# Kernel optimization log

Measured on AMD Instinct MI355X. Metric: run time of the kernel, lower is better.

## Reference

```python
import jax, jax.numpy as jnp
import numpy as np

N, E, H, L, IN_DIM, OUT_DIM = 50000, 500000, 128, 6, 3, 9


def _lin_init(k, fi, fo):
    W = jax.random.normal(k, (fi, fo), jnp.float32) / np.sqrt(fi)
    return W, jnp.zeros((fo,), jnp.float32)


def setup_inputs() -> dict:
    key = jax.random.key(0)
    ks = jax.random.split(key, 40)
    inp = {}
    inp['x'] = jax.random.normal(ks[0], (N, IN_DIM), jnp.float32)
    inp['coords'] = jax.random.uniform(ks[1], (N, 3), jnp.float32)
    inp['edge_index'] = jax.random.randint(ks[2], (2, E), 0, N, jnp.int64)
    # encoders
    inp['W_ne1'], inp['b_ne1'] = _lin_init(ks[3], IN_DIM, H)
    inp['W_ne2'], inp['b_ne2'] = _lin_init(ks[4], H, H)
    inp['W_ee1'], inp['b_ee1'] = _lin_init(ks[5], 4, H)
    inp['W_ee2'], inp['b_ee2'] = _lin_init(ks[6], H, H)
    # per-layer params, stacked over L
    def stack(fn):
        Ws, bs = zip(*[fn(l) for l in range(L)])
        return jnp.stack(Ws), jnp.stack(bs)
    inp['We1'], inp['be1'] = stack(lambda l: _lin_init(ks[7 + l], 3 * H, H))
    inp['We2'], inp['be2'] = stack(lambda l: _lin_init(ks[13 + l], H, H))
    inp['Wn1'], inp['bn1'] = stack(lambda l: _lin_init(ks[19 + l], 2 * H, H))
    inp['Wn2'], inp['bn2'] = stack(lambda l: _lin_init(ks[25 + l], H, H))
    inp['ln_g'] = jnp.ones((L, H), jnp.float32)
    inp['ln_b'] = jnp.zeros((L, H), jnp.float32)
    # decoder
    inp['Wd1'], inp['bd1'] = _lin_init(ks[31], H, H)
    inp['Wd2'], inp['bd2'] = _lin_init(ks[32], H, OUT_DIM)
    return inp


def _mlp2(x, W1, b1, W2, b2):
    return jax.nn.silu(x @ W1 + b1) @ W2 + b2


def _layernorm(x, g, b, eps=1e-5):
    m = jnp.mean(x, -1, keepdims=True)
    v = jnp.mean(jnp.square(x - m), -1, keepdims=True)
    return (x - m) / jnp.sqrt(v + eps) * g + b


def reference(x, coords, edge_index,
              W_ne1, b_ne1, W_ne2, b_ne2, W_ee1, b_ee1, W_ee2, b_ee2,
              We1, be1, We2, be2, Wn1, bn1, Wn2, bn2, ln_g, ln_b,
              Wd1, bd1, Wd2, bd2):
    src, dst = edge_index[0], edge_index[1]
    # edge features: relative displacement + distance -> (E,4)
    rel = coords[dst] - coords[src]
    ef = jnp.concatenate([rel, jnp.linalg.norm(rel, axis=-1, keepdims=True)], -1)
    edge_attr = _mlp2(ef, W_ee1, b_ee1, W_ee2, b_ee2)  # (E,H)
    h = _mlp2(x, W_ne1, b_ne1, W_ne2, b_ne2)           # (N,H)
    # in-degree for mean aggregation (PyG mean -> 0 for isolated nodes)
    deg = jax.ops.segment_sum(jnp.ones((E,), h.dtype), dst, num_segments=N)
    denom = jnp.maximum(deg, 1.0)[:, None]
    for l in range(L):
        # message: phi_e(x_i=h[dst], x_j=h[src], e_ij)
        m_in = jnp.concatenate([h[dst], h[src], edge_attr], -1)  # (E,3H)
        msg = _mlp2(m_in, We1[l], be1[l], We2[l], be2[l])        # (E,H)
        agg = jax.ops.segment_sum(msg, dst, num_segments=N) / denom
        upd = _mlp2(jnp.concatenate([h, agg], -1), Wn1[l], bn1[l], Wn2[l], bn2[l])
        h = _layernorm(upd + h, ln_g[l], ln_b[l])
    return _mlp2(h, Wd1, bd1, Wd2, bd2)  # (N,out_dim)
```

## Files before the change

kernel.cpp:

```cpp
#include <hip/hip_runtime.h>

#define NN 50000
#define NE 500000
#define HD 128

typedef _Float16 f16;
typedef _Float16 f16x8 __attribute__((ext_vector_type(8)));
typedef _Float16 f16x4 __attribute__((ext_vector_type(4)));
typedef float f32x4 __attribute__((ext_vector_type(4)));


__device__ __forceinline__ int swz(int r, int c) {
  return r * HD + ((((c >> 3) ^ r) & 15) << 3) + (c & 7);
}

__device__ __forceinline__ float fast_silu(float x) {
  return x * __builtin_amdgcn_rcpf(1.0f + __expf(-x));
}

__device__ __forceinline__ void gemm_wave_g(const f16* A, const f16* __restrict__ Wg,
                                            int wstride, int rowBase, int colBase,
                                            f32x4 acc[2][4]) {
  const int lane = (int)threadIdx.x & 63;
  const int m = lane & 15;
  const int q = lane >> 4;
#pragma unroll
  for (int kc = 0; kc < 4; ++kc) {
    const int pc = (((kc * 4 + q) ^ m) & 15) << 3;
    const int gk = (kc * 4 + q) << 3;
    f16x8 a0 = *(const f16x8*)(A + (rowBase + m) * HD + pc);
    f16x8 a1 = *(const f16x8*)(A + (rowBase + 16 + m) * HD + pc);
#pragma unroll
    for (int ct = 0; ct < 4; ++ct) {
      f16x8 b = *(const f16x8*)(Wg + (colBase + ct * 16 + m) * wstride + gk);
      acc[0][ct] = __builtin_amdgcn_mfma_f32_16x16x32_f16(a0, b, acc[0][ct], 0, 0, 0);
      acc[1][ct] = __builtin_amdgcn_mfma_f32_16x16x32_f16(a1, b, acc[1][ct], 0, 0, 0);
    }
  }
}

__device__ __forceinline__ void gemm_wave_g2(const f16* A, const f16* __restrict__ Wg,
                                             int wstride, int rowBase, int colBase,
                                             f32x4 acc[2][2]) {
  const int lane = (int)threadIdx.x & 63;
  const int m = lane & 15;
  const int q = lane >> 4;
#pragma unroll
  for (int kc = 0; kc < 4; ++kc) {
    const int pc = (((kc * 4 + q) ^ m) & 15) << 3;
    const int gk = (kc * 4 + q) << 3;
    f16x8 a0 = *(const f16x8*)(A + (rowBase + m) * HD + pc);
    f16x8 a1 = *(const f16x8*)(A + (rowBase + 16 + m) * HD + pc);
#pragma unroll
    for (int ct = 0; ct < 2; ++ct) {
      f16x8 b = *(const f16x8*)(Wg + (colBase + ct * 16 + m) * wstride + gk);
      acc[0][ct] = __builtin_amdgcn_mfma_f32_16x16x32_f16(a0, b, acc[0][ct], 0, 0, 0);
      acc[1][ct] = __builtin_amdgcn_mfma_f32_16x16x32_f16(a1, b, acc[1][ct], 0, 0, 0);
    }
  }
}

#define ZACC(acc)                                        \
  {                                                      \
    _Pragma("unroll") for (int zi = 0; zi < 2; ++zi)     \
        _Pragma("unroll") for (int zj = 0; zj < 4; ++zj) \
            acc[zi][zj] = (f32x4){0.f, 0.f, 0.f, 0.f};   \
  }

#define ZACC2(acc)                                       \
  {                                                      \
    _Pragma("unroll") for (int zi = 0; zi < 2; ++zi)     \
        _Pragma("unroll") for (int zj = 0; zj < 2; ++zj) \
            acc[zi][zj] = (f32x4){0.f, 0.f, 0.f, 0.f};   \
  }

template <int TPB>
__device__ __forceinline__ void stage_rows64(const f16* __restrict__ g, long r0,
                                             long lim, f16* lds) {
#pragma unroll
  for (int it = 0; it < 1024 / TPB; ++it) {
    int idx = it * TPB + (int)threadIdx.x;
    int r = idx >> 4, ck = idx & 15;
    f16x8 v = {};
    if (r0 + r < lim) v = *(const f16x8*)(g + (r0 + r) * HD + ck * 8);
    *(f16x8*)(lds + r * HD + (((ck ^ r) & 15) << 3)) = v;
  }
}
template <int TPB>
__device__ __forceinline__ void store_rows64(const f16* lds, f16* __restrict__ g,
                                             long r0, long lim) {
#pragma unroll
  for (int it = 0; it < 1024 / TPB; ++it) {
    int idx = it * TPB + (int)threadIdx.x;
    int r = idx >> 4, ck = idx & 15;
    if (r0 + r < lim)
      *(f16x8*)(g + (r0 + r) * HD + ck * 8) =
          *(const f16x8*)(lds + r * HD + (((ck ^ r) & 15) << 3));
  }
}

struct TJob {
  const float* src;
  f16* dst;
  int idim;
  int odim;
};
struct TJobs {
  TJob j[27];
};

__global__ __launch_bounds__(256) void k_prep(TJobs jobs) {
  int job = blockIdx.x >> 2;
  int part = blockIdx.x & 3;
  TJob J = jobs.j[job];
  int total = J.idim * J.odim;
  for (int idx = part * 256 + (int)threadIdx.x; idx < total; idx += 1024) {
    int o = idx / J.idim;
    int i = idx - o * J.idim;
    J.dst[idx] = (f16)J.src[(long)i * J.odim + o];
  }
}

__global__ __launch_bounds__(128) void k_prep_E(const float* __restrict__ W,
                                                f16* __restrict__ W8) {
  int t = threadIdx.x;
#pragma unroll
  for (int i = 0; i < 8; ++i) W8[t * 8 + i] = (i < 4) ? (f16)W[i * 128 + t] : (f16)0.f;
}

__global__ __launch_bounds__(128) void k_prep_M(const float* __restrict__ Wee2,
                                                const float* __restrict__ b2,
                                                const float* __restrict__ We1,
                                                f16* __restrict__ Mt,
                                                float* __restrict__ cv) {
  __shared__ float col[128];
  int l = blockIdx.x >> 7, o = blockIdx.x & 127;
  int t = threadIdx.x;
  col[t] = We1[((size_t)l * 384 + 256 + t) * 128 + o];
  __syncthreads();
  float s = 0.f;
#pragma unroll 8
  for (int e = 0; e < 128; ++e) s += Wee2[t * 128 + e] * col[e];
  Mt[((size_t)l * 128 + o) * 128 + t] = (f16)s;
  if (t == 0) {
    float c = 0.f;
    for (int e = 0; e < 128; ++e) c += b2[e] * col[e];
    cv[l * 128 + o] = c;
  }
}

__global__ __launch_bounds__(128) void k_prep_Z(const float* __restrict__ We2,
                                                const float* __restrict__ be2,
                                                const float* __restrict__ Wn1,
                                                f16* __restrict__ WZt,
                                                float* __restrict__ bve) {
  __shared__ float col[128];
  int l = blockIdx.x >> 7, o = blockIdx.x & 127;
  int t = threadIdx.x;
  col[t] = Wn1[((size_t)l * 256 + 128 + t) * 128 + o];
  __syncthreads();
  float s = 0.f;
#pragma unroll 8
  for (int j = 0; j < 128; ++j) s += We2[(size_t)l * 128 * 128 + t * 128 + j] * col[j];
  WZt[((size_t)l * 128 + o) * 128 + t] = (f16)s;
  if (t == 0) {
    float c = 0.f;
    for (int j = 0; j < 128; ++j) c += be2[l * 128 + j] * col[j];
    bve[l * 128 + o] = c;
  }
}

__global__ __launch_bounds__(256) void k_hist(const int* __restrict__ dst,
                                              int* __restrict__ count) {
  int e = blockIdx.x * 256 + threadIdx.x;
  if (e < NE) atomicAdd(&count[dst[e]], 1);
}

__global__ __launch_bounds__(1024) void k_scan(const int* __restrict__ count,
                                               int* __restrict__ startA) {
  __shared__ int lds[1024];
  const int CH = 49;
  int t = threadIdx.x;
  int b = t * CH;
  int e = b + CH < NN ? b + CH : NN;
  int s = 0;
  for (int i = b; i < e; ++i) s += count[i];
  lds[t] = s;
  __syncthreads();
  for (int off = 1; off < 1024; off <<= 1) {
    int v = (t >= off) ? lds[t - off] : 0;
    __syncthreads();
    lds[t] += v;
    __syncthreads();
  }
  int run = lds[t] - s;
  for (int i = b; i < e; ++i) {
    startA[i] = run;
    run += count[i];
  }
  if (t == 0) startA[NN] = NE;
}

__global__ __launch_bounds__(256) void k_scatter(const int* __restrict__ src,
                                                 const int* __restrict__ dst,
                                                 const float* __restrict__ coords,
                                                 const int* __restrict__ startA,
                                                 int* __restrict__ cursor,
                                                 int* __restrict__ srcS,
                                                 int* __restrict__ dstS,
                                                 f16* __restrict__ efS) {
  int e = blockIdx.x * 256 + threadIdx.x;
  if (e >= NE) return;
  int s = src[e];
  int n = dst[e];
  int pos = startA[n] + atomicAdd(&cursor[n], 1);
  srcS[pos] = s;
  dstS[pos] = n;
  float rx = coords[n * 3] - coords[s * 3];
  float ry = coords[n * 3 + 1] - coords[s * 3 + 1];
  float rz = coords[n * 3 + 2] - coords[s * 3 + 2];
  float nr = sqrtf(rx * rx + ry * ry + rz * rz);
  f16x8 v = {};
  v[0] = (f16)rx;
  v[1] = (f16)ry;
  v[2] = (f16)rz;
  v[3] = (f16)nr;
  *(f16x8*)(efS + (long)pos * 8) = v;
}

__global__ __launch_bounds__(256, 4) void k_enc_node(
    const float* __restrict__ x, const float* __restrict__ W1,
    const float* __restrict__ b1, const f16* __restrict__ W2t,
    const float* __restrict__ b2, float* __restrict__ h32, f16* __restrict__ h16) {
  __shared__ __align__(16) f16 lds_A[64 * HD];
  __shared__ __align__(16) f16 lds_O[64 * HD];
  float* lds_x = (float*)lds_O;
  long r0 = (long)blockIdx.x * 64;
  int t = threadIdx.x;
  int wv = t >> 6, lane = t & 63, nn = lane & 15, q = lane >> 4;
  int rowBase = (wv >> 1) * 32, colBase = (wv & 1) * 64;

  if (t < 192) {
    long i = r0 * 3 + t;
    lds_x[t] = (i < (long)NN * 3) ? x[i] : 0.f;
  }
  __syncthreads();

  for (int it = 0; it < 32; ++it) {
    int idx = it * 256 + t;
    int r = idx >> 7, c = idx & 127;
    float a = b1[c];
    a += lds_x[r * 3 + 0] * W1[0 * HD + c];
    a += lds_x[r * 3 + 1] * W1[1 * HD + c];
    a += lds_x[r * 3 + 2] * W1[2 * HD + c];
    lds_A[swz(r, c)] = (f16)fast_silu(a);
  }
  __syncthreads();

  f32x4 acc[2][4];
  ZACC(acc);
  gemm_wave_g(lds_A, W2t, HD, rowBase, colBase, acc);
#pragma unroll
  for (int rt = 0; rt < 2; ++rt)
#pragma unroll
    for (int ct = 0; ct < 4; ++ct)
#pragma unroll
      for (int rg = 0; rg < 4; ++rg) {
        int row = rowBase + rt * 16 + q * 4 + rg;
        int col = colBase + ct * 16 + nn;
        float v = acc[rt][ct][rg] + b2[col];
        long nr = r0 + row;
        if (nr < NN) h32[nr * HD + col] = v;
        lds_O[swz(row, col)] = (f16)v;
      }
  __syncthreads();
  store_rows64<256>(lds_O, h16, r0, NN);
}

__global__ __launch_bounds__(512, 8) void k_pp(const f16* __restrict__ h16,
                                               const f16* __restrict__ We1t,
                                               const float* __restrict__ be1,
                                               const float* __restrict__ cvec,
                                               f16* __restrict__ Pd,
                                               f16* __restrict__ Ps) {
  __shared__ __align__(16) f16 lds_A[64 * HD];
  __shared__ __align__(16) f16 lds_O[64 * HD];
  long r0 = (long)blockIdx.x * 64;
  int t = threadIdx.x;
  int wv = t >> 6, lane = t & 63, nn = lane & 15, q = lane >> 4;
  int rowBase = (wv >> 2) * 32, colBase = (wv & 3) * 32;

  stage_rows64<512>(h16, r0, NN, lds_A);
  __syncthreads();

  f32x4 acc[2][2];
  ZACC2(acc);
  gemm_wave_g2(lds_A, We1t, 384, rowBase, colBase, acc);
#pragma unroll
  for (int rt = 0; rt < 2; ++rt)
#pragma unroll
    for (int ct = 0; ct < 2; ++ct)
#pragma unroll
      for (int rg = 0; rg < 4; ++rg) {
        int row = rowBase + rt * 16 + q * 4 + rg;
        int col = colBase + ct * 16 + nn;
        lds_O[swz(row, col)] = (f16)(acc[rt][ct][rg] + be1[col] + cvec[col]);
      }
  __syncthreads();
  store_rows64<512>(lds_O, Pd, r0, NN);

  ZACC2(acc);
  gemm_wave_g2(lds_A, We1t + 128, 384, rowBase, colBase, acc);
  __syncthreads();
#pragma unroll
  for (int rt = 0; rt < 2; ++rt)
#pragma unroll
    for (int ct = 0; ct < 2; ++ct)
#pragma unroll
      for (int rg = 0; rg < 4; ++rg) {
        int row = rowBase + rt * 16 + q * 4 + rg;
        int col = colBase + ct * 16 + nn;
        lds_O[swz(row, col)] = (f16)acc[rt][ct][rg];
      }
  __syncthreads();
  store_rows64<512>(lds_O, Ps, r0, NN);
}

__global__ __launch_bounds__(512, 8) void k_edge(
    const f16* __restrict__ efS, const int* __restrict__ srcS,
    const int* __restrict__ dstS, const f16* __restrict__ Pd,
    const f16* __restrict__ Ps, const f16* __restrict__ W1e8,
    const float* __restrict__ b1, const f16* __restrict__ Mt,
    float* __restrict__ zs, int nwg) {
  __shared__ __align__(16) f16 lds_A[64 * HD];
  __shared__ __align__(16) f16 lds_P[64 * HD];
  __shared__ int dstL[64];
  int orig = blockIdx.x;
  int xcd = orig & 7, loc = orig >> 3;
  int qq = nwg >> 3, rr = nwg & 7;
  int wg = (xcd < rr ? xcd * (qq + 1) : rr * (qq + 1) + (xcd - rr) * qq) + loc;
  long e0 = (long)wg * 64;
  int t = threadIdx.x;
  int lane = t & 63, nn = lane & 15, q = lane >> 4;
  int wv = t >> 6;
  int rowBase = (wv >> 2) * 32, colBase = (wv & 3) * 32;

  if (t < 64) {
    long e = e0 + t;
    dstL[t] = (e < NE) ? dstS[e] : -1;
  }

  f16x8 ea0 = {}, ea1 = {}, eb0 = {}, eb1 = {};
  if (q == 0) {
    long er0 = e0 + rowBase + nn;
    long er1 = er0 + 16;
    if (er0 < NE) ea0 = *(const f16x8*)(efS + er0 * 8);
    if (er1 < NE) ea1 = *(const f16x8*)(efS + er1 * 8);
    eb0 = *(const f16x8*)(W1e8 + (colBase + nn) * 8);
    eb1 = *(const f16x8*)(W1e8 + (colBase + 16 + nn) * 8);
  }
  f32x4 sacc[2][2];
  ZACC2(sacc);
  sacc[0][0] = __builtin_amdgcn_mfma_f32_16x16x32_f16(ea0, eb0, sacc[0][0], 0, 0, 0);
  sacc[1][0] = __builtin_amdgcn_mfma_f32_16x16x32_f16(ea1, eb0, sacc[1][0], 0, 0, 0);
  sacc[0][1] = __builtin_amdgcn_mfma_f32_16x16x32_f16(ea0, eb1, sacc[0][1], 0, 0, 0);
  sacc[1][1] = __builtin_amdgcn_mfma_f32_16x16x32_f16(ea1, eb1, sacc[1][1], 0, 0, 0);

  int rr0 = t >> 4, rr1 = 32 + (t >> 4);
  int ck = t & 15;
  f16x8 pa0 = {}, pb0 = {}, pa1 = {}, pb1 = {};
  {
    long e = e0 + rr0;
    if (e < NE) {
      int d = dstS[e], s = srcS[e];
      pa0 = *(const f16x8*)(Pd + (long)d * HD + ck * 8);
      pb0 = *(const f16x8*)(Ps + (long)s * HD + ck * 8);
    }
  }
  {
    long e = e0 + rr1;
    if (e < NE) {
      int d = dstS[e], s = srcS[e];
      pa1 = *(const f16x8*)(Pd + (long)d * HD + ck * 8);
      pb1 = *(const f16x8*)(Ps + (long)s * HD + ck * 8);
    }
  }

  {
    float b1v0 = b1[colBase + nn], b1v1 = b1[colBase + 16 + nn];
#pragma unroll
    for (int rt = 0; rt < 2; ++rt)
#pragma unroll
      for (int ct = 0; ct < 2; ++ct) {
        float bb = ct ? b1v1 : b1v0;
        int col = colBase + ct * 16 + nn;
#pragma unroll
        for (int rg = 0; rg < 4; ++rg) {
          int row = rowBase + rt * 16 + q * 4 + rg;
          lds_A[swz(row, col)] = (f16)fast_silu(sacc[rt][ct][rg] + bb);
        }
      }
  }
  {
    f16x8 v = pa0 + pb0;
    *(f16x8*)(lds_P + rr0 * HD + (((ck ^ rr0) & 15) << 3)) = v;
  }
  {
    f16x8 v = pa1 + pb1;
    *(f16x8*)(lds_P + rr1 * HD + (((ck ^ rr1) & 15) << 3)) = v;
  }
  __syncthreads();

  f32x4 acc[2][2];
  ZACC2(acc);
  gemm_wave_g2(lds_A, Mt, HD, rowBase, colBase, acc);

#pragma unroll
  for (int rt = 0; rt < 2; ++rt)
#pragma unroll
    for (int ct = 0; ct < 2; ++ct)
#pragma unroll
      for (int rg = 0; rg < 4; ++rg) {
        int row = rowBase + rt * 16 + q * 4 + rg;
        int col = colBase + ct * 16 + nn;
        float v = acc[rt][ct][rg] + (float)lds_P[swz(row, col)];
        lds_P[swz(row, col)] = (f16)fast_silu(v);
      }
  __syncthreads();

  {
    int c = t & 127, qt = t >> 7;
    int rb = qt * 16;
    int dfirst = dstL[rb], dlast = dstL[rb + 15];
    int prev = dfirst;
    float sum = 0.f;
    for (int r = rb; r < rb + 16; ++r) {
      int d = dstL[r];
      if (d != prev) {
        if (prev >= 0) {
          if (prev == dfirst || prev == dlast)
            atomicAdd(&zs[(long)prev * HD + c], sum);
          else
            zs[(long)prev * HD + c] = sum;
        }
        sum = 0.f;
        prev = d;
      }
      sum += (float)lds_P[swz(r, c)];
    }
    if (prev >= 0) atomicAdd(&zs[(long)prev * HD + c], sum);
  }
}

__global__ __launch_bounds__(256, 4) void k_node(
    const f16* __restrict__ h16in, float* __restrict__ zsum,
    const int* __restrict__ startA, const f16* __restrict__ Wn1t,
    const float* __restrict__ bn1, const f16* __restrict__ WZt,
    const float* __restrict__ bve, const f16* __restrict__ Wn2t,
    const float* __restrict__ bn2, const float* __restrict__ lg,
    const float* __restrict__ lb, float* __restrict__ h32,
    f16* __restrict__ h16out) {
  __shared__ __align__(16) f16 lds_A[64 * HD];
  __shared__ __align__(16) f16 lds_B[64 * HD];
  __shared__ float lds_s[512];
  __shared__ float degf[64];
  long r0 = (long)blockIdx.x * 64;
  int t = threadIdx.x;
  int wv = t >> 6, lane = t & 63, nn = lane & 15, q = lane >> 4;
  int rowBase = (wv >> 1) * 32, colBase = (wv & 1) * 64;

  stage_rows64<256>(h16in, r0, NN, lds_A);
#pragma unroll
  for (int it = 0; it < 8; ++it) {
    int idx = it * 256 + t;
    int r = idx >> 5, c4 = (idx & 31) * 4;
    long nr = r0 + r;
    f16x4 v = {};
    if (nr < NN) {
      float deg = (float)(startA[nr + 1] - startA[nr]);
      float inv = __builtin_amdgcn_rcpf(fmaxf(deg, 1.0f));
      float4 a = *(const float4*)(zsum + nr * HD + c4);
      *(float4*)(zsum + nr * HD + c4) = (float4){0.f, 0.f, 0.f, 0.f};
      v[0] = (f16)(a.x * inv);
      v[1] = (f16)(a.y * inv);
      v[2] = (f16)(a.z * inv);
      v[3] = (f16)(a.w * inv);
      if (c4 == 0) degf[r] = deg > 0.f ? 1.f : 0.f;
    } else if (c4 == 0) {
      degf[r] = 0.f;
    }
    *(f16x4*)(lds_B + swz(r, c4)) = v;
  }
  __syncthreads();

  f32x4 acc[2][4];
  ZACC(acc);
  gemm_wave_g(lds_A, Wn1t, 256, rowBase, colBase, acc);
  gemm_wave_g(lds_B, WZt, HD, rowBase, colBase, acc);
  __syncthreads();

#pragma unroll
  for (int rt = 0; rt < 2; ++rt)
#pragma unroll
    for (int ct = 0; ct < 4; ++ct)
#pragma unroll
      for (int rg = 0; rg < 4; ++rg) {
        int row = rowBase + rt * 16 + q * 4 + rg;
        int col = colBase + ct * 16 + nn;
        lds_B[swz(row, col)] =
            (f16)fast_silu(acc[rt][ct][rg] + bn1[col] + degf[row] * bve[col]);
      }
  __syncthreads();

  ZACC(acc);
  gemm_wave_g(lds_B, Wn2t, HD, rowBase, colBase, acc);

  float vv[2][4][4];
  float s1[8], s2[8];
#pragma unroll
  for (int i = 0; i < 8; ++i) {
    s1[i] = 0.f;
    s2[i] = 0.f;
  }
#pragma unroll
  for (int rt = 0; rt < 2; ++rt)
#pragma unroll
    for (int ct = 0; ct < 4; ++ct)
#pragma unroll
      for (int rg = 0; rg < 4; ++rg) {
        int row = rowBase + rt * 16 + q * 4 + rg;
        int col = colBase + ct * 16 + nn;
        long nr = r0 + row;
        float hv = (nr < NN) ? h32[nr * HD + col] : 0.f;
        float v = acc[rt][ct][rg] + bn2[col] + hv;
        vv[rt][ct][rg] = v;
        s1[rt * 4 + rg] += v;
        s2[rt * 4 + rg] += v * v;
      }
#pragma unroll
  for (int msk = 1; msk <= 8; msk <<= 1) {
#pragma unroll
    for (int i = 0; i < 8; ++i) {
      s1[i] += __shfl_xor(s1[i], msk, 64);
      s2[i] += __shfl_xor(s2[i], msk, 64);
    }
  }
  int ch = wv & 1;
  if (nn == 0) {
#pragma unroll
    for (int rt = 0; rt < 2; ++rt)
#pragma unroll
      for (int rg = 0; rg < 4; ++rg) {
        int row = rowBase + rt * 16 + q * 4 + rg;
        lds_s[row * 2 + ch] = s1[rt * 4 + rg];
        lds_s[256 + row * 2 + ch] = s2[rt * 4 + rg];
      }
  }
  __syncthreads();
#pragma unroll
  for (int rt = 0; rt < 2; ++rt)
#pragma unroll
    for (int ct = 0; ct < 4; ++ct)
#pragma unroll
      for (int rg = 0; rg < 4; ++rg) {
        int row = rowBase + rt * 16 + q * 4 + rg;
        int col = colBase + ct * 16 + nn;
        long nr = r0 + row;
        float S1 = lds_s[row * 2] + lds_s[row * 2 + 1];
        float S2 = lds_s[256 + row * 2] + lds_s[256 + row * 2 + 1];
        float mean = S1 * (1.0f / 128.0f);
        float var = S2 * (1.0f / 128.0f) - mean * mean;
        float rstd = rsqrtf(var + 1e-5f);
        float y = (vv[rt][ct][rg] - mean) * rstd * lg[col] + lb[col];
        if (nr < NN) h32[nr * HD + col] = y;
        lds_A[swz(row, col)] = (f16)y;
      }
  __syncthreads();
  store_rows64<256>(lds_A, h16out, r0, NN);
}

__global__ __launch_bounds__(256, 4) void k_dec(
    const f16* __restrict__ h16, const f16* __restrict__ Wd1t,
    const float* __restrict__ bd1, const float* __restrict__ Wd2,
    const float* __restrict__ bd2, float* __restrict__ out) {
  __shared__ __align__(16) f16 lds_A[64 * HD];
  __shared__ __align__(16) f16 lds_O[64 * HD];
  long r0 = (long)blockIdx.x * 64;
  int t = threadIdx.x;
  int wv = t >> 6, lane = t & 63, nn = lane & 15, q = lane >> 4;
  int rowBase = (wv >> 1) * 32, colBase = (wv & 1) * 64;

  stage_rows64<256>(h16, r0, NN, lds_A);
  __syncthreads();

  f32x4 acc[2][4];
  ZACC(acc);
  gemm_wave_g(lds_A, Wd1t, HD, rowBase, colBase, acc);
#pragma unroll
  for (int rt = 0; rt < 2; ++rt)
#pragma unroll
    for (int ct = 0; ct < 4; ++ct)
#pragma unroll
      for (int rg = 0; rg < 4; ++rg) {
        int row = rowBase + rt * 16 + q * 4 + rg;
        int col = colBase + ct * 16 + nn;
        lds_O[swz(row, col)] = (f16)fast_silu(acc[rt][ct][rg] + bd1[col]);
      }
  __syncthreads();

  for (int idx = t; idx < 64 * 9; idx += 256) {
    int r = idx / 9;
    int o = idx - r * 9;
    long nr = r0 + r;
    if (nr < NN) {
      float a = bd2[o];
      for (int k = 0; k < 128; ++k) a += (float)lds_O[swz(r, k)] * Wd2[k * 9 + o];
      out[nr * 9 + o] = a;
    }
  }
}

extern "C" void kernel_launch(void* const* d_in, const int* in_sizes, int n_in,
                              void* d_out, int out_size, void* d_ws, size_t ws_size,
                              hipStream_t stream) {
  (void)in_sizes;
  (void)n_in;
  (void)out_size;
  (void)ws_size;
  const float* x = (const float*)d_in[0];
  const float* coords = (const float*)d_in[1];
  const int* ei = (const int*)d_in[2];
  const float* W_ne1 = (const float*)d_in[3];
  const float* b_ne1 = (const float*)d_in[4];
  const float* W_ne2 = (const float*)d_in[5];
  const float* b_ne2 = (const float*)d_in[6];
  const float* W_ee1 = (const float*)d_in[7];
  const float* b_ee1 = (const float*)d_in[8];
  const float* W_ee2 = (const float*)d_in[9];
  const float* b_ee2 = (const float*)d_in[10];
  const float* We1 = (const float*)d_in[11];
  const float* be1 = (const float*)d_in[12];
  const float* We2 = (const float*)d_in[13];
  const float* be2 = (const float*)d_in[14];
  const float* Wn1 = (const float*)d_in[15];
  const float* bn1 = (const float*)d_in[16];
  const float* Wn2 = (const float*)d_in[17];
  const float* bn2 = (const float*)d_in[18];
  const float* ln_g = (const float*)d_in[19];
  const float* ln_b = (const float*)d_in[20];
  const float* Wd1 = (const float*)d_in[21];
  const float* bd1 = (const float*)d_in[22];
  const float* Wd2 = (const float*)d_in[23];
  const float* bd2 = (const float*)d_in[24];
  float* out = (float*)d_out;

  char* ws = (char*)d_ws;
  size_t off = 0;
  auto alloc = [&](size_t bytes) -> void* {
    void* p = ws + off;
    off = (off + bytes + 255) & ~(size_t)255;
    return p;
  };
  float* h32 = (float*)alloc((size_t)NN * HD * 4);
  f16* h16 = (f16*)alloc((size_t)NN * HD * 2);
  f16* Pd = (f16*)alloc((size_t)NN * HD * 2);
  f16* Ps = (f16*)alloc((size_t)NN * HD * 2);
  float* agg = (float*)alloc((size_t)NN * HD * 4);
  f16* efS = (f16*)alloc((size_t)NE * 8 * 2);
  int* srcS = (int*)alloc((size_t)NE * 4);
  int* dstS = (int*)alloc((size_t)NE * 4);
  int* count = (int*)alloc((size_t)2 * NN * 4);
  int* cursor = count + NN;
  int* startA = (int*)alloc((size_t)(NN + 1) * 4);
  f16* wt_ne2 = (f16*)alloc(128 * 128 * 2);
  f16* we1t = (f16*)alloc((size_t)6 * 128 * 384 * 2);
  f16* wn1t = (f16*)alloc((size_t)6 * 128 * 256 * 2);
  f16* wn2t = (f16*)alloc((size_t)6 * 128 * 128 * 2);
  f16* wd1t = (f16*)alloc(128 * 128 * 2);
  f16* mt = (f16*)alloc((size_t)6 * 128 * 128 * 2);
  float* cvec = (float*)alloc((size_t)6 * 128 * 4);
  f16* wzt = (f16*)alloc((size_t)6 * 128 * 128 * 2);
  float* bvv = (float*)alloc((size_t)6 * 128 * 4);
  f16* w1e8 = (f16*)alloc(128 * 8 * 2);

  TJobs jobs;
  int nj = 0;
  jobs.j[nj++] = {W_ne2, wt_ne2, 128, 128};
  for (int l = 0; l < 6; ++l)
    jobs.j[nj++] = {We1 + (size_t)l * 384 * 128, we1t + (size_t)l * 128 * 384, 384, 128};
  for (int l = 0; l < 6; ++l)
    jobs.j[nj++] = {Wn1 + (size_t)l * 256 * 128, wn1t + (size_t)l * 128 * 256, 256, 128};
  for (int l = 0; l < 6; ++l)
    jobs.j[nj++] = {Wn2 + (size_t)l * 128 * 128, wn2t + (size_t)l * 128 * 128, 128, 128};
  jobs.j[nj++] = {Wd1, wd1t, 128, 128};

  const int* srcI = ei;
  const int* dstI = ei + NE;
  const int EB = (NE + 255) / 256;
  const int NT = (NN + 63) / 64;
  const int ET = (NE + 63) / 64;

  k_prep<<<nj * 4, 256, 0, stream>>>(jobs);
  k_prep_E<<<1, 128, 0, stream>>>(W_ee1, w1e8);
  k_prep_M<<<6 * 128, 128, 0, stream>>>(W_ee2, b_ee2, We1, mt, cvec);
  k_prep_Z<<<6 * 128, 128, 0, stream>>>(We2, be2, Wn1, wzt, bvv);
  hipMemsetAsync(count, 0, (size_t)2 * NN * 4, stream);
  hipMemsetAsync(agg, 0, (size_t)NN * HD * 4, stream);
  k_hist<<<EB, 256, 0, stream>>>(dstI, count);
  k_scan<<<1, 1024, 0, stream>>>(count, startA);
  k_scatter<<<EB, 256, 0, stream>>>(srcI, dstI, coords, startA, cursor, srcS, dstS, efS);
  k_enc_node<<<NT, 256, 0, stream>>>(x, W_ne1, b_ne1, wt_ne2, b_ne2, h32, h16);

  for (int l = 0; l < 6; ++l) {
    k_pp<<<NT, 512, 0, stream>>>(h16, we1t + (size_t)l * 128 * 384, be1 + l * 128,
                                 cvec + l * 128, Pd, Ps);
    k_edge<<<ET, 512, 0, stream>>>(efS, srcS, dstS, Pd, Ps, w1e8, b_ee1,
                                   mt + (size_t)l * 128 * 128, agg, ET);
    k_node<<<NT, 256, 0, stream>>>(h16, agg, startA, wn1t + (size_t)l * 128 * 256,
                                   bn1 + l * 128, wzt + (size_t)l * 128 * 128,
                                   bvv + l * 128, wn2t + (size_t)l * 128 * 128,
                                   bn2 + l * 128, ln_g + l * 128, ln_b + l * 128, h32, h16);
  }
  k_dec<<<NT, 256, 0, stream>>>(h16, wd1t, bd1, Wd2, bd2, out);
}
```

Baseline: 1.323 ms.

## Fuse per-layer node projection into node update and encoder kernels

Removes the standalone k_pp launch by computing the next layer's Pd/Ps projections at the end of k_node, and the first layer's inside k_enc_node, reusing the freshly computed h tile already in LDS. k_node is also re-tiled from 256 to 512 threads with 4 column-waves, and the LayerNorm partial-sum reduction is adjusted to match. This saves six kernel launches and a re-read of h16 from global memory per layer. In exchange k_node gets heavier, with more registers and LDS traffic per block, which may lower occupancy.

```diff
diff --git a/kernel.cpp b/kernel.cpp
--- a/kernel.cpp
+++ b/kernel.cpp
@@ -231,7 +231,10 @@
 __global__ __launch_bounds__(256, 4) void k_enc_node(
     const float* __restrict__ x, const float* __restrict__ W1,
     const float* __restrict__ b1, const f16* __restrict__ W2t,
-    const float* __restrict__ b2, float* __restrict__ h32, f16* __restrict__ h16) {
+    const float* __restrict__ b2, const f16* __restrict__ We1t0,
+    const float* __restrict__ be10, const float* __restrict__ cvec0,
+    float* __restrict__ h32, f16* __restrict__ h16, f16* __restrict__ Pd,
+    f16* __restrict__ Ps) {
   __shared__ __align__(16) f16 lds_A[64 * HD];
   __shared__ __align__(16) f16 lds_O[64 * HD];
   float* lds_x = (float*)lds_O;
@@ -275,55 +278,37 @@
       }
   __syncthreads();
   store_rows64<256>(lds_O, h16, r0, NN);
-}
-
-__global__ __launch_bounds__(512, 8) void k_pp(const f16* __restrict__ h16,
-                                               const f16* __restrict__ We1t,
-                                               const float* __restrict__ be1,
-                                               const float* __restrict__ cvec,
-                                               f16* __restrict__ Pd,
-                                               f16* __restrict__ Ps) {
-  __shared__ __align__(16) f16 lds_A[64 * HD];
-  __shared__ __align__(16) f16 lds_O[64 * HD];
-  long r0 = (long)blockIdx.x * 64;
-  int t = threadIdx.x;
-  int wv = t >> 6, lane = t & 63, nn = lane & 15, q = lane >> 4;
-  int rowBase = (wv >> 2) * 32, colBase = (wv & 3) * 32;
-
-  stage_rows64<512>(h16, r0, NN, lds_A);
-  __syncthreads();
-
-  f32x4 acc[2][2];
-  ZACC2(acc);
-  gemm_wave_g2(lds_A, We1t, 384, rowBase, colBase, acc);
+
+  ZACC(acc);
+  gemm_wave_g(lds_O, We1t0, 384, rowBase, colBase, acc);
 #pragma unroll
   for (int rt = 0; rt < 2; ++rt)
 #pragma unroll
-    for (int ct = 0; ct < 2; ++ct)
-#pragma unroll
-      for (int rg = 0; rg < 4; ++rg) {
-        int row = rowBase + rt * 16 + q * 4 + rg;
-        int col = colBase + ct * 16 + nn;
-        lds_O[swz(row, col)] = (f16)(acc[rt][ct][rg] + be1[col] + cvec[col]);
-      }
-  __syncthreads();
-  store_rows64<512>(lds_O, Pd, r0, NN);
-
-  ZACC2(acc);
-  gemm_wave_g2(lds_A, We1t + 128, 384, rowBase, colBase, acc);
+    for (int ct = 0; ct < 4; ++ct)
+#pragma unroll
+      for (int rg = 0; rg < 4; ++rg) {
+        int row = rowBase + rt * 16 + q * 4 + rg;
+        int col = colBase + ct * 16 + nn;
+        lds_A[swz(row, col)] = (f16)(acc[rt][ct][rg] + be10[col] + cvec0[col]);
+      }
+  __syncthreads();
+  store_rows64<256>(lds_A, Pd, r0, NN);
+
+  ZACC(acc);
+  gemm_wave_g(lds_O, We1t0 + 128, 384, rowBase, colBase, acc);
   __syncthreads();
 #pragma unroll
   for (int rt = 0; rt < 2; ++rt)
 #pragma unroll
-    for (int ct = 0; ct < 2; ++ct)
-#pragma unroll
-      for (int rg = 0; rg < 4; ++rg) {
-        int row = rowBase + rt * 16 + q * 4 + rg;
-        int col = colBase + ct * 16 + nn;
-        lds_O[swz(row, col)] = (f16)acc[rt][ct][rg];
-      }
-  __syncthreads();
-  store_rows64<512>(lds_O, Ps, r0, NN);
+    for (int ct = 0; ct < 4; ++ct)
+#pragma unroll
+      for (int rg = 0; rg < 4; ++rg) {
+        int row = rowBase + rt * 16 + q * 4 + rg;
+        int col = colBase + ct * 16 + nn;
+        lds_A[swz(row, col)] = (f16)acc[rt][ct][rg];
+      }
+  __syncthreads();
+  store_rows64<256>(lds_A, Ps, r0, NN);
 }
 
 __global__ __launch_bounds__(512, 8) void k_edge(
@@ -452,14 +437,16 @@
   }
 }
 
-__global__ __launch_bounds__(256, 4) void k_node(
+__global__ __launch_bounds__(512, 6) void k_node(
     const f16* __restrict__ h16in, float* __restrict__ zsum,
     const int* __restrict__ startA, const f16* __restrict__ Wn1t,
     const float* __restrict__ bn1, const f16* __restrict__ WZt,
     const float* __restrict__ bve, const f16* __restrict__ Wn2t,
     const float* __restrict__ bn2, const float* __restrict__ lg,
-    const float* __restrict__ lb, float* __restrict__ h32,
-    f16* __restrict__ h16out) {
+    const float* __restrict__ lb, const f16* __restrict__ We1tN,
+    const float* __restrict__ be1N, const float* __restrict__ cvecN,
+    float* __restrict__ h32, f16* __restrict__ h16out, f16* __restrict__ Pd,
+    f16* __restrict__ Ps, int doPP) {
   __shared__ __align__(16) f16 lds_A[64 * HD];
   __shared__ __align__(16) f16 lds_B[64 * HD];
   __shared__ float lds_s[512];
@@ -467,12 +454,12 @@
   long r0 = (long)blockIdx.x * 64;
   int t = threadIdx.x;
   int wv = t >> 6, lane = t & 63, nn = lane & 15, q = lane >> 4;
-  int rowBase = (wv >> 1) * 32, colBase = (wv & 1) * 64;
-
-  stage_rows64<256>(h16in, r0, NN, lds_A);
-#pragma unroll
-  for (int it = 0; it < 8; ++it) {
-    int idx = it * 256 + t;
+  int rowBase = (wv >> 2) * 32, colBase = (wv & 3) * 32;
+
+  stage_rows64<512>(h16in, r0, NN, lds_A);
+#pragma unroll
+  for (int it = 0; it < 4; ++it) {
+    int idx = it * 512 + t;
     int r = idx >> 5, c4 = (idx & 31) * 4;
     long nr = r0 + r;
     f16x4 v = {};
@@ -493,16 +480,16 @@
   }
   __syncthreads();
 
-  f32x4 acc[2][4];
-  ZACC(acc);
-  gemm_wave_g(lds_A, Wn1t, 256, rowBase, colBase, acc);
-  gemm_wave_g(lds_B, WZt, HD, rowBase, colBase, acc);
+  f32x4 acc[2][2];
+  ZACC2(acc);
+  gemm_wave_g2(lds_A, Wn1t, 256, rowBase, colBase, acc);
+  gemm_wave_g2(lds_B, WZt, HD, rowBase, colBase, acc);
   __syncthreads();
 
 #pragma unroll
   for (int rt = 0; rt < 2; ++rt)
 #pragma unroll
-    for (int ct = 0; ct < 4; ++ct)
+    for (int ct = 0; ct < 2; ++ct)
 #pragma unroll
       for (int rg = 0; rg < 4; ++rg) {
         int row = rowBase + rt * 16 + q * 4 + rg;
@@ -512,10 +499,10 @@
       }
   __syncthreads();
 
-  ZACC(acc);
-  gemm_wave_g(lds_B, Wn2t, HD, rowBase, colBase, acc);
-
-  float vv[2][4][4];
+  ZACC2(acc);
+  gemm_wave_g2(lds_B, Wn2t, HD, rowBase, colBase, acc);
+
+  float vv[2][2][4];
   float s1[8], s2[8];
 #pragma unroll
   for (int i = 0; i < 8; ++i) {
@@ -525,7 +512,7 @@
 #pragma unroll
   for (int rt = 0; rt < 2; ++rt)
 #pragma unroll
-    for (int ct = 0; ct < 4; ++ct)
+    for (int ct = 0; ct < 2; ++ct)
 #pragma unroll
       for (int rg = 0; rg < 4; ++rg) {
         int row = rowBase + rt * 16 + q * 4 + rg;
@@ -545,29 +532,31 @@
       s2[i] += __shfl_xor(s2[i], msk, 64);
     }
   }
-  int ch = wv & 1;
+  int ch = wv & 3;
   if (nn == 0) {
 #pragma unroll
     for (int rt = 0; rt < 2; ++rt)
 #pragma unroll
       for (int rg = 0; rg < 4; ++rg) {
         int row = rowBase + rt * 16 + q * 4 + rg;
-        lds_s[row * 2 + ch] = s1[rt * 4 + rg];
-        lds_s[256 + row * 2 + ch] = s2[rt * 4 + rg];
+        lds_s[row * 4 + ch] = s1[rt * 4 + rg];
+        lds_s[256 + row * 4 + ch] = s2[rt * 4 + rg];
       }
   }
   __syncthreads();
 #pragma unroll
   for (int rt = 0; rt < 2; ++rt)
 #pragma unroll
-    for (int ct = 0; ct < 4; ++ct)
+    for (int ct = 0; ct < 2; ++ct)
 #pragma unroll
       for (int rg = 0; rg < 4; ++rg) {
         int row = rowBase + rt * 16 + q * 4 + rg;
         int col = colBase + ct * 16 + nn;
         long nr = r0 + row;
-        float S1 = lds_s[row * 2] + lds_s[row * 2 + 1];
-        float S2 = lds_s[256 + row * 2] + lds_s[256 + row * 2 + 1];
+        float S1 = lds_s[row * 4] + lds_s[row * 4 + 1] + lds_s[row * 4 + 2] +
+                   lds_s[row * 4 + 3];
+        float S2 = lds_s[256 + row * 4] + lds_s[256 + row * 4 + 1] +
+                   lds_s[256 + row * 4 + 2] + lds_s[256 + row * 4 + 3];
         float mean = S1 * (1.0f / 128.0f);
         float var = S2 * (1.0f / 128.0f) - mean * mean;
         float rstd = rsqrtf(var + 1e-5f);
@@ -576,7 +565,40 @@
         lds_A[swz(row, col)] = (f16)y;
       }
   __syncthreads();
-  store_rows64<256>(lds_A, h16out, r0, NN);
+  store_rows64<512>(lds_A, h16out, r0, NN);
+
+  if (doPP) {
+    ZACC2(acc);
+    gemm_wave_g2(lds_A, We1tN, 384, rowBase, colBase, acc);
+#pragma unroll
+    for (int rt = 0; rt < 2; ++rt)
+#pragma unroll
+      for (int ct = 0; ct < 2; ++ct)
+#pragma unroll
+        for (int rg = 0; rg < 4; ++rg) {
+          int row = rowBase + rt * 16 + q * 4 + rg;
+          int col = colBase + ct * 16 + nn;
+          lds_B[swz(row, col)] = (f16)(acc[rt][ct][rg] + be1N[col] + cvecN[col]);
+        }
+    __syncthreads();
+    store_rows64<512>(lds_B, Pd, r0, NN);
+
+    ZACC2(acc);
+    gemm_wave_g2(lds_A, We1tN + 128, 384, rowBase, colBase, acc);
+    __syncthreads();
+#pragma unroll
+    for (int rt = 0; rt < 2; ++rt)
+#pragma unroll
+      for (int ct = 0; ct < 2; ++ct)
+#pragma unroll
+        for (int rg = 0; rg < 4; ++rg) {
+          int row = rowBase + rt * 16 + q * 4 + rg;
+          int col = colBase + ct * 16 + nn;
+          lds_B[swz(row, col)] = (f16)acc[rt][ct][rg];
+        }
+    __syncthreads();
+    store_rows64<512>(lds_B, Ps, r0, NN);
+  }
 }
 
 __global__ __launch_bounds__(256, 4) void k_dec(
@@ -709,17 +731,19 @@
   k_hist<<<EB, 256, 0, stream>>>(dstI, count);
   k_scan<<<1, 1024, 0, stream>>>(count, startA);
   k_scatter<<<EB, 256, 0, stream>>>(srcI, dstI, coords, startA, cursor, srcS, dstS, efS);
-  k_enc_node<<<NT, 256, 0, stream>>>(x, W_ne1, b_ne1, wt_ne2, b_ne2, h32, h16);
+  k_enc_node<<<NT, 256, 0, stream>>>(x, W_ne1, b_ne1, wt_ne2, b_ne2, we1t, be1, cvec,
+                                     h32, h16, Pd, Ps);
 
   for (int l = 0; l < 6; ++l) {
-    k_pp<<<NT, 512, 0, stream>>>(h16, we1t + (size_t)l * 128 * 384, be1 + l * 128,
-                                 cvec + l * 128, Pd, Ps);
+    int ln = (l + 1 < 6) ? (l + 1) : 0;
     k_edge<<<ET, 512, 0, stream>>>(efS, srcS, dstS, Pd, Ps, w1e8, b_ee1,
                                    mt + (size_t)l * 128 * 128, agg, ET);
-    k_node<<<NT, 256, 0, stream>>>(h16, agg, startA, wn1t + (size_t)l * 128 * 256,
-                                   bn1 + l * 128, wzt + (size_t)l * 128 * 128,
-                                   bvv + l * 128, wn2t + (size_t)l * 128 * 128,
-                                   bn2 + l * 128, ln_g + l * 128, ln_b + l * 128, h32, h16);
+    k_node<<<NT, 512, 0, stream>>>(
+        h16, agg, startA, wn1t + (size_t)l * 128 * 256, bn1 + l * 128,
+        wzt + (size_t)l * 128 * 128, bvv + l * 128, wn2t + (size_t)l * 128 * 128,
+        bn2 + l * 128, ln_g + l * 128, ln_b + l * 128,
+        we1t + (size_t)ln * 128 * 384, be1 + ln * 128, cvec + ln * 128, h32, h16,
+        Pd, Ps, (l + 1 < 6) ? 1 : 0);
   }
   k_dec<<<NT, 256, 0, stream>>>(h16, wd1t, bd1, Wd2, bd2, out);
 }
```

Result: slower. 1.458 ms (+10.3%).
